# Performance work log

Measured on AMD Instinct MI355X. Metric: run time of the kernel, lower is better.

Reference implementation:

```python
import jax, jax.numpy as jnp
import numpy as np
import math

N_WIRES = 8

def _cnot(state, ctrl, tgt):
    # state: (N, 2,2,...,2) with wire w on axis 1+w
    c_ax = 1 + ctrl
    t_ax = 1 + tgt
    s0 = jnp.take(state, 0, axis=c_ax)
    s1 = jnp.take(state, 1, axis=c_ax)
    t2 = t_ax - 1 if t_ax > c_ax else t_ax
    s1 = jnp.flip(s1, axis=t2)
    return jnp.stack([s0, s1], axis=c_ax)

def _qlayer(x, phi):
    # x: (N, 8) encoder RX angles; phi: (8,) trainable RX angles.
    # encoder RX(x_i) followed by RX(phi_i) on the same wire == RX(x_i + phi_i)
    N = x.shape[0]
    half = 0.5 * (x + phi)
    c = jnp.cos(half).astype(jnp.complex64)
    s = jnp.sin(half).astype(jnp.complex64)
    amp = jnp.stack([c, (-1j) * s], axis=-1)  # (N, 8, 2) per-wire RX|0>
    # product state via successive outer products -> (N, 2,...,2)
    state = amp[:, 0]
    for w in range(1, N_WIRES):
        q = amp[:, w].reshape((N,) + (1,) * w + (2,))
        state = state[..., None] * q
    # CNOT ring
    for w in range(N_WIRES - 1):
        state = _cnot(state, w, w + 1)
    state = _cnot(state, N_WIRES - 1, 0)
    probs = state.real ** 2 + state.imag ** 2  # (N, 2,...,2)
    exps = []
    for w in range(N_WIRES):
        axes = tuple(a for a in range(1, N_WIRES + 1) if a != 1 + w)
        pw = jnp.sum(probs, axis=axes)  # (N, 2)
        exps.append(pw[:, 0] - pw[:, 1])  # <Z_w>
    return jnp.stack(exps, axis=-1)  # (N, 8)


def setup_inputs() -> dict:
    key = jax.random.key(0)
    k1, k2, k3 = jax.random.split(key, 3)
    B, S, E = 4, 1024, 128
    x = jax.random.normal(k1, (B, S, E), jnp.float32)
    phi = jax.random.normal(k2, (N_WIRES,), jnp.float32)
    W = jax.random.normal(k3, (E, E), jnp.float32) / math.sqrt(E)
    b = jnp.zeros((E,), jnp.float32)
    return {"x": x, "phi": phi, "W": W, "b": b}


def reference(x, phi, W, b):
    B, S, E = x.shape
    H = 16
    d = N_WIRES  # head dim == n_wires == 8
    xh = x.reshape(B, S, H, d).reshape(-1, d)
    proj = _qlayer(xh, phi).reshape(B, S, H, d)
    # q, k, v are identical (same layer, same input, deterministic) -> compute once
    q = jnp.transpose(proj, (0, 2, 1, 3))  # (B, H, S, d)
    scores = jnp.einsum('bhqd,bhkd->bhqk', q, q) / math.sqrt(d)
    attn = jax.nn.softmax(scores, axis=-1)  # dropout: eval mode (identity)
    out = jnp.einsum('bhqk,bhkd->bhqd', attn, q)
    out = jnp.transpose(out, (0, 2, 1, 3)).reshape(B, S, E)
    return out @ W.T + b
```

## Files before the change

### kernel.cpp

```cpp
#include <hip/hip_runtime.h>

#define NB 4
#define NS 1024
#define NE 128
#define NH 16
#define ND 8

typedef __attribute__((ext_vector_type(4))) _Float16 half4v;
typedef __attribute__((ext_vector_type(8))) _Float16 half8v;
typedef __attribute__((ext_vector_type(2))) _Float16 half2v;
typedef __attribute__((ext_vector_type(4))) float float4v;

#if __has_builtin(__builtin_amdgcn_exp2f)
#define EXP2F(x) __builtin_amdgcn_exp2f(x)
#else
#define EXP2F(x) __expf(0.69314718055994531f * (x))
#endif

#define SQRT_ALPHA 0.71423656f

__global__ __launch_bounds__(1024, 8)
void qattn_kernel(const float* __restrict__ x, const float* __restrict__ phi,
                  float* __restrict__ aout)
{
    __shared__ __align__(16) _Float16 Klds[NS][8];
    __shared__ __align__(16) _Float16 Vt[9][1036];
    __shared__ __align__(16) float4 scratch[8][64];

    const int t    = threadIdx.x;
    const int blk  = blockIdx.x;
    const int qt   = blk & 7;
    const int bh   = blk >> 3;
    const int b    = bh >> 4;
    const int h    = bh & 15;
    const int lane = t & 63;
    const int w    = t >> 6;
    const int qsub = w & 7;
    const int kh   = w >> 3;

    const float ph0 = phi[0], ph1 = phi[1], ph2 = phi[2], ph3 = phi[3];
    const float ph4 = phi[4], ph5 = phi[5], ph6 = phi[6], ph7 = phi[7];

    {
        const int k = t;
        const float* xr = x + ((size_t)(b * NS + k)) * NE + h * ND;
        float4 xa = *(const float4*)xr;
        float4 xc = *(const float4*)(xr + 4);
        float g0 = __cosf(xa.x + ph0), g1 = __cosf(xa.y + ph1);
        float g2 = __cosf(xa.z + ph2), g3 = __cosf(xa.w + ph3);
        float g4 = __cosf(xc.x + ph4), g5 = __cosf(xc.y + ph5);
        float g6 = __cosf(xc.z + ph6), g7 = __cosf(xc.w + ph7);
        float s7 = g7, s6 = s7 * g6, s5 = s6 * g5, s4 = s5 * g4, s3 = s4 * g3, s2 = s3 * g2;
        float v0 = s2 * g1;
        float v1 = g0 * g1, v2 = v1 * g2, v3 = v2 * g3;
        float v4 = v3 * g4, v5 = v4 * g5, v6 = v5 * g6, v7 = v6 * g7;
        half8v row;
        row[0] = (_Float16)(SQRT_ALPHA * v0); row[1] = (_Float16)(SQRT_ALPHA * v1);
        row[2] = (_Float16)(SQRT_ALPHA * v2); row[3] = (_Float16)(SQRT_ALPHA * v3);
        row[4] = (_Float16)(SQRT_ALPHA * v4); row[5] = (_Float16)(SQRT_ALPHA * v5);
        row[6] = (_Float16)(SQRT_ALPHA * v6); row[7] = (_Float16)(SQRT_ALPHA * v7);
        *(half8v*)&Klds[k][0] = row;
        Vt[0][k] = (_Float16)v0; Vt[1][k] = (_Float16)v1;
        Vt[2][k] = (_Float16)v2; Vt[3][k] = (_Float16)v3;
        Vt[4][k] = (_Float16)v4; Vt[5][k] = (_Float16)v5;
        Vt[6][k] = (_Float16)v6; Vt[7][k] = (_Float16)v7;
        Vt[8][k] = (_Float16)1.0f;
    }
    __syncthreads();

    const int e = lane & 15;
    const int g = lane >> 4;

    half4v qf = (half4v)(_Float16)0.0f;
    if (lane < 32) {
        int qrow = qt * 128 + qsub * 16 + e;
        qf = *(const half4v*)&Klds[qrow][g * 4];
    }

    const _Float16* kp = &Klds[kh * 512 + e][(g & 1) * 4];
    const int ecl = (e > 8) ? 8 : e;
    const _Float16* vp = &Vt[ecl][kh * 512 + g * 4];

    float4v acc = (float4v)0.0f;
    const float4v zero = (float4v)0.0f;

    for (int batch = 0; batch < 8; ++batch) {
        const _Float16* kpb = kp + batch * 512;
        const _Float16* vpb = vp + batch * 64;

        half4v kf0 = *(const half4v*)(kpb);
        half4v kf1 = *(const half4v*)(kpb + 128);
        half4v kf2 = *(const half4v*)(kpb + 256);
        half4v kf3 = *(const half4v*)(kpb + 384);
        half4v vf0 = *(const half4v*)(vpb);
        half4v vf1 = *(const half4v*)(vpb + 16);
        half4v vf2 = *(const half4v*)(vpb + 32);
        half4v vf3 = *(const half4v*)(vpb + 48);

        float4v s0 = __builtin_amdgcn_mfma_f32_16x16x16f16(kf0, qf, zero, 0, 0, 0);
        float4v s1 = __builtin_amdgcn_mfma_f32_16x16x16f16(kf1, qf, zero, 0, 0, 0);
        float4v s2 = __builtin_amdgcn_mfma_f32_16x16x16f16(kf2, qf, zero, 0, 0, 0);
        float4v s3 = __builtin_amdgcn_mfma_f32_16x16x16f16(kf3, qf, zero, 0, 0, 0);

        float p00 = EXP2F(s0[0]), p01 = EXP2F(s0[1]), p02 = EXP2F(s0[2]), p03 = EXP2F(s0[3]);
        float p10 = EXP2F(s1[0]), p11 = EXP2F(s1[1]), p12 = EXP2F(s1[2]), p13 = EXP2F(s1[3]);
        float p20 = EXP2F(s2[0]), p21 = EXP2F(s2[1]), p22 = EXP2F(s2[2]), p23 = EXP2F(s2[3]);
        float p30 = EXP2F(s3[0]), p31 = EXP2F(s3[1]), p32 = EXP2F(s3[2]), p33 = EXP2F(s3[3]);

        half2v lo0 = __builtin_bit_cast(half2v, __builtin_amdgcn_cvt_pkrtz(p00, p01));
        half2v hi0 = __builtin_bit_cast(half2v, __builtin_amdgcn_cvt_pkrtz(p02, p03));
        half2v lo1 = __builtin_bit_cast(half2v, __builtin_amdgcn_cvt_pkrtz(p10, p11));
        half2v hi1 = __builtin_bit_cast(half2v, __builtin_amdgcn_cvt_pkrtz(p12, p13));
        half2v lo2 = __builtin_bit_cast(half2v, __builtin_amdgcn_cvt_pkrtz(p20, p21));
        half2v hi2 = __builtin_bit_cast(half2v, __builtin_amdgcn_cvt_pkrtz(p22, p23));
        half2v lo3 = __builtin_bit_cast(half2v, __builtin_amdgcn_cvt_pkrtz(p30, p31));
        half2v hi3 = __builtin_bit_cast(half2v, __builtin_amdgcn_cvt_pkrtz(p32, p33));
        half4v pa0 = __builtin_shufflevector(lo0, hi0, 0, 1, 2, 3);
        half4v pa1 = __builtin_shufflevector(lo1, hi1, 0, 1, 2, 3);
        half4v pa2 = __builtin_shufflevector(lo2, hi2, 0, 1, 2, 3);
        half4v pa3 = __builtin_shufflevector(lo3, hi3, 0, 1, 2, 3);

        acc = __builtin_amdgcn_mfma_f32_16x16x16f16(pa0, vf0, acc, 0, 0, 0);
        acc = __builtin_amdgcn_mfma_f32_16x16x16f16(pa1, vf1, acc, 0, 0, 0);
        acc = __builtin_amdgcn_mfma_f32_16x16x16f16(pa2, vf2, acc, 0, 0, 0);
        acc = __builtin_amdgcn_mfma_f32_16x16x16f16(pa3, vf3, acc, 0, 0, 0);
    }

    if (kh == 1) {
        scratch[qsub][lane] = make_float4(acc[0], acc[1], acc[2], acc[3]);
    }
    __syncthreads();
    if (kh == 0) {
        float4 c = scratch[qsub][lane];
        acc[0] += c.x; acc[1] += c.y; acc[2] += c.z; acc[3] += c.w;

        const int src = (lane & 48) | 8;
        float d0 = __shfl(acc[0], src, 64);
        float d1 = __shfl(acc[1], src, 64);
        float d2 = __shfl(acc[2], src, 64);
        float d3 = __shfl(acc[3], src, 64);
        float o0 = acc[0] / d0, o1 = acc[1] / d1;
        float o2 = acc[2] / d2, o3 = acc[3] / d3;
        if (e < 8) {
            size_t rbase = (size_t)(b * NS + qt * 128 + qsub * 16 + g * 4);
            float* op = aout + rbase * NE + h * ND + e;
            op[0 * NE] = o0;
            op[1 * NE] = o1;
            op[2 * NE] = o2;
            op[3 * NE] = o3;
        }
    }
}

__global__ __launch_bounds__(512)
void proj_kernel(const float* __restrict__ A, const float* __restrict__ W,
                 const float* __restrict__ bias, float* __restrict__ out)
{
    __shared__ float Wt[64][NE + 4];
    __shared__ float As[16][NE];

    const int t  = threadIdx.x;
    const int r0 = blockIdx.x * 16;

    for (int i = t; i < 16 * NE; i += 512) {
        As[i >> 7][i & 127] = A[(size_t)(r0 + (i >> 7)) * NE + (i & 127)];
    }

    const int c4 = (t & 31) * 4;
    const int rg = t >> 5;
    float acc0 = 0, acc1 = 0, acc2 = 0, acc3 = 0;

    for (int eh = 0; eh < 2; ++eh) {
        if (eh) __syncthreads();
        for (int i = t; i < NE * 64; i += 512) {
            int c = i >> 6;
            int e = i & 63;
            Wt[e][c] = W[c * NE + eh * 64 + e];
        }
        __syncthreads();
#pragma unroll 8
        for (int e = 0; e < 64; ++e) {
            float4 wv = *(const float4*)&Wt[e][c4];
            float av = As[rg][eh * 64 + e];
            acc0 += av * wv.x; acc1 += av * wv.y;
            acc2 += av * wv.z; acc3 += av * wv.w;
        }
    }

    float4 bv = *(const float4*)&bias[c4];
    float4 o = make_float4(acc0 + bv.x, acc1 + bv.y, acc2 + bv.z, acc3 + bv.w);
    *(float4*)(out + (size_t)(r0 + rg) * NE + c4) = o;
}

extern "C" void kernel_launch(void* const* d_in, const int* in_sizes, int n_in,
                              void* d_out, int out_size, void* d_ws, size_t ws_size,
                              hipStream_t stream)
{
    (void)in_sizes; (void)n_in; (void)out_size; (void)d_ws; (void)ws_size;
    const float* x   = (const float*)d_in[0];
    const float* phi = (const float*)d_in[1];
    const float* W   = (const float*)d_in[2];
    const float* b   = (const float*)d_in[3];
    float* out = (float*)d_out;

    qattn_kernel<<<dim3(NB * NH * 8), dim3(1024), 0, stream>>>(x, phi, out);
    proj_kernel<<<dim3(NB * NS / 16), dim3(512), 0, stream>>>(out, W, b, out);
}
```

Before: 24.09 us.

## Halve attention block size and reuse each K/V fragment across four query tiles

The attention kernel now runs 512 threads per block. Each wave handles four 16-row query tiles and one quarter of the keys, so every K and V fragment loaded from LDS feeds four MFMAs instead of one. Each thread computes two key rows in the encoder prologue, and the partial sums from the four key-split waves are combined in two shared-memory reduction steps. This cuts LDS traffic per MFMA but needs more registers per thread and one extra barrier, and each block now has half the waves available to hide latency.

New measurement: 24.86 us. 3.2% more time.

```diff
diff --git a/kernel.cpp b/kernel.cpp
--- a/kernel.cpp
+++ b/kernel.cpp
@@ -19,13 +19,13 @@
 
 #define SQRT_ALPHA 0.71423656f
 
-__global__ __launch_bounds__(1024, 8)
+__global__ __launch_bounds__(512, 4)
 void qattn_kernel(const float* __restrict__ x, const float* __restrict__ phi,
                   float* __restrict__ aout)
 {
     __shared__ __align__(16) _Float16 Klds[NS][8];
     __shared__ __align__(16) _Float16 Vt[9][1036];
-    __shared__ __align__(16) float4 scratch[8][64];
+    __shared__ __align__(16) float4 scratch[2][2][4][64];
 
     const int t    = threadIdx.x;
     const int blk  = blockIdx.x;
@@ -35,72 +35,81 @@
     const int h    = bh & 15;
     const int lane = t & 63;
     const int w    = t >> 6;
-    const int qsub = w & 7;
-    const int kh   = w >> 3;
+    const int qg   = w & 1;
+    const int kh   = w >> 1;
 
     const float ph0 = phi[0], ph1 = phi[1], ph2 = phi[2], ph3 = phi[3];
     const float ph4 = phi[4], ph5 = phi[5], ph6 = phi[6], ph7 = phi[7];
 
     {
-        const int k = t;
-        const float* xr = x + ((size_t)(b * NS + k)) * NE + h * ND;
-        float4 xa = *(const float4*)xr;
-        float4 xc = *(const float4*)(xr + 4);
-        float g0 = __cosf(xa.x + ph0), g1 = __cosf(xa.y + ph1);
-        float g2 = __cosf(xa.z + ph2), g3 = __cosf(xa.w + ph3);
-        float g4 = __cosf(xc.x + ph4), g5 = __cosf(xc.y + ph5);
-        float g6 = __cosf(xc.z + ph6), g7 = __cosf(xc.w + ph7);
-        float s7 = g7, s6 = s7 * g6, s5 = s6 * g5, s4 = s5 * g4, s3 = s4 * g3, s2 = s3 * g2;
-        float v0 = s2 * g1;
-        float v1 = g0 * g1, v2 = v1 * g2, v3 = v2 * g3;
-        float v4 = v3 * g4, v5 = v4 * g5, v6 = v5 * g6, v7 = v6 * g7;
-        half8v row;
-        row[0] = (_Float16)(SQRT_ALPHA * v0); row[1] = (_Float16)(SQRT_ALPHA * v1);
-        row[2] = (_Float16)(SQRT_ALPHA * v2); row[3] = (_Float16)(SQRT_ALPHA * v3);
-        row[4] = (_Float16)(SQRT_ALPHA * v4); row[5] = (_Float16)(SQRT_ALPHA * v5);
-        row[6] = (_Float16)(SQRT_ALPHA * v6); row[7] = (_Float16)(SQRT_ALPHA * v7);
-        *(half8v*)&Klds[k][0] = row;
-        Vt[0][k] = (_Float16)v0; Vt[1][k] = (_Float16)v1;
-        Vt[2][k] = (_Float16)v2; Vt[3][k] = (_Float16)v3;
-        Vt[4][k] = (_Float16)v4; Vt[5][k] = (_Float16)v5;
-        Vt[6][k] = (_Float16)v6; Vt[7][k] = (_Float16)v7;
-        Vt[8][k] = (_Float16)1.0f;
+        const float* xb = x + ((size_t)b * NS) * NE + h * ND;
+        const int k0 = t, k1 = t + 512;
+        float4 xa0 = *(const float4*)(xb + (size_t)k0 * NE);
+        float4 xc0 = *(const float4*)(xb + (size_t)k0 * NE + 4);
+        float4 xa1 = *(const float4*)(xb + (size_t)k1 * NE);
+        float4 xc1 = *(const float4*)(xb + (size_t)k1 * NE + 4);
+#pragma unroll
+        for (int half = 0; half < 2; ++half) {
+            const int k = half ? k1 : k0;
+            const float4 xa = half ? xa1 : xa0;
+            const float4 xc = half ? xc1 : xc0;
+            float g0 = __cosf(xa.x + ph0), g1 = __cosf(xa.y + ph1);
+            float g2 = __cosf(xa.z + ph2), g3 = __cosf(xa.w + ph3);
+            float g4 = __cosf(xc.x + ph4), g5 = __cosf(xc.y + ph5);
+            float g6 = __cosf(xc.z + ph6), g7 = __cosf(xc.w + ph7);
+            float s7 = g7, s6 = s7 * g6, s5 = s6 * g5, s4 = s5 * g4, s3 = s4 * g3, s2 = s3 * g2;
+            float v0 = s2 * g1;
+            float v1 = g0 * g1, v2 = v1 * g2, v3 = v2 * g3;
+            float v4 = v3 * g4, v5 = v4 * g5, v6 = v5 * g6, v7 = v6 * g7;
+            half8v row;
+            row[0] = (_Float16)(SQRT_ALPHA * v0); row[1] = (_Float16)(SQRT_ALPHA * v1);
+            row[2] = (_Float16)(SQRT_ALPHA * v2); row[3] = (_Float16)(SQRT_ALPHA * v3);
+            row[4] = (_Float16)(SQRT_ALPHA * v4); row[5] = (_Float16)(SQRT_ALPHA * v5);
+            row[6] = (_Float16)(SQRT_ALPHA * v6); row[7] = (_Float16)(SQRT_ALPHA * v7);
+            *(half8v*)&Klds[k][0] = row;
+            Vt[0][k] = (_Float16)v0; Vt[1][k] = (_Float16)v1;
+            Vt[2][k] = (_Float16)v2; Vt[3][k] = (_Float16)v3;
+            Vt[4][k] = (_Float16)v4; Vt[5][k] = (_Float16)v5;
+            Vt[6][k] = (_Float16)v6; Vt[7][k] = (_Float16)v7;
+            Vt[8][k] = (_Float16)1.0f;
+        }
     }
     __syncthreads();
 
     const int e = lane & 15;
     const int g = lane >> 4;
 
-    half4v qf = (half4v)(_Float16)0.0f;
+    half4v qf0 = (half4v)(_Float16)0.0f;
+    half4v qf1 = (half4v)(_Float16)0.0f;
+    half4v qf2 = (half4v)(_Float16)0.0f;
+    half4v qf3 = (half4v)(_Float16)0.0f;
     if (lane < 32) {
-        int qrow = qt * 128 + qsub * 16 + e;
-        qf = *(const half4v*)&Klds[qrow][g * 4];
-    }
-
-    const _Float16* kp = &Klds[kh * 512 + e][(g & 1) * 4];
+        const int qbase = qt * 128 + qg * 64 + e;
+        qf0 = *(const half4v*)&Klds[qbase][g * 4];
+        qf1 = *(const half4v*)&Klds[qbase + 16][g * 4];
+        qf2 = *(const half4v*)&Klds[qbase + 32][g * 4];
+        qf3 = *(const half4v*)&Klds[qbase + 48][g * 4];
+    }
+
+    const _Float16* kp = &Klds[kh * 256 + e][(g & 1) * 4];
     const int ecl = (e > 8) ? 8 : e;
-    const _Float16* vp = &Vt[ecl][kh * 512 + g * 4];
-
-    float4v acc = (float4v)0.0f;
+    const _Float16* vp = &Vt[ecl][kh * 256 + g * 4];
+
+    float4v acc0 = (float4v)0.0f;
+    float4v acc1 = (float4v)0.0f;
+    float4v acc2 = (float4v)0.0f;
+    float4v acc3 = (float4v)0.0f;
     const float4v zero = (float4v)0.0f;
 
-    for (int batch = 0; batch < 8; ++batch) {
-        const _Float16* kpb = kp + batch * 512;
-        const _Float16* vpb = vp + batch * 64;
-
-        half4v kf0 = *(const half4v*)(kpb);
-        half4v kf1 = *(const half4v*)(kpb + 128);
-        half4v kf2 = *(const half4v*)(kpb + 256);
-        half4v kf3 = *(const half4v*)(kpb + 384);
-        half4v vf0 = *(const half4v*)(vpb);
-        half4v vf1 = *(const half4v*)(vpb + 16);
-        half4v vf2 = *(const half4v*)(vpb + 32);
-        half4v vf3 = *(const half4v*)(vpb + 48);
-
-        float4v s0 = __builtin_amdgcn_mfma_f32_16x16x16f16(kf0, qf, zero, 0, 0, 0);
-        float4v s1 = __builtin_amdgcn_mfma_f32_16x16x16f16(kf1, qf, zero, 0, 0, 0);
-        float4v s2 = __builtin_amdgcn_mfma_f32_16x16x16f16(kf2, qf, zero, 0, 0, 0);
-        float4v s3 = __builtin_amdgcn_mfma_f32_16x16x16f16(kf3, qf, zero, 0, 0, 0);
+#pragma unroll 4
+    for (int tt = 0; tt < 16; ++tt) {
+        half4v kf = *(const half4v*)(kp + tt * 128);
+        half4v vf = *(const half4v*)(vp + tt * 16);
+
+        float4v s0 = __builtin_amdgcn_mfma_f32_16x16x16f16(kf, qf0, zero, 0, 0, 0);
+        float4v s1 = __builtin_amdgcn_mfma_f32_16x16x16f16(kf, qf1, zero, 0, 0, 0);
+        float4v s2 = __builtin_amdgcn_mfma_f32_16x16x16f16(kf, qf2, zero, 0, 0, 0);
+        float4v s3 = __builtin_amdgcn_mfma_f32_16x16x16f16(kf, qf3, zero, 0, 0, 0);
 
         float p00 = EXP2F(s0[0]), p01 = EXP2F(s0[1]), p02 = EXP2F(s0[2]), p03 = EXP2F(s0[3]);
         float p10 = EXP2F(s1[0]), p11 = EXP2F(s1[1]), p12 = EXP2F(s1[2]), p13 = EXP2F(s1[3]);
@@ -115,39 +124,69 @@
         half2v hi2 = __builtin_bit_cast(half2v, __builtin_amdgcn_cvt_pkrtz(p22, p23));
         half2v lo3 = __builtin_bit_cast(half2v, __builtin_amdgcn_cvt_pkrtz(p30, p31));
         half2v hi3 = __builtin_bit_cast(half2v, __builtin_amdgcn_cvt_pkrtz(p32, p33));
+
         half4v pa0 = __builtin_shufflevector(lo0, hi0, 0, 1, 2, 3);
         half4v pa1 = __builtin_shufflevector(lo1, hi1, 0, 1, 2, 3);
         half4v pa2 = __builtin_shufflevector(lo2, hi2, 0, 1, 2, 3);
         half4v pa3 = __builtin_shufflevector(lo3, hi3, 0, 1, 2, 3);
 
-        acc = __builtin_amdgcn_mfma_f32_16x16x16f16(pa0, vf0, acc, 0, 0, 0);
-        acc = __builtin_amdgcn_mfma_f32_16x16x16f16(pa1, vf1, acc, 0, 0, 0);
-        acc = __builtin_amdgcn_mfma_f32_16x16x16f16(pa2, vf2, acc, 0, 0, 0);
-        acc = __builtin_amdgcn_mfma_f32_16x16x16f16(pa3, vf3, acc, 0, 0, 0);
-    }
-
+        acc0 = __builtin_amdgcn_mfma_f32_16x16x16f16(pa0, vf, acc0, 0, 0, 0);
+        acc1 = __builtin_amdgcn_mfma_f32_16x16x16f16(pa1, vf, acc1, 0, 0, 0);
+        acc2 = __builtin_amdgcn_mfma_f32_16x16x16f16(pa2, vf, acc2, 0, 0, 0);
+        acc3 = __builtin_amdgcn_mfma_f32_16x16x16f16(pa3, vf, acc3, 0, 0, 0);
+    }
+
+    if (kh >= 2) {
+        scratch[kh - 2][qg][0][lane] = make_float4(acc0[0], acc0[1], acc0[2], acc0[3]);
+        scratch[kh - 2][qg][1][lane] = make_float4(acc1[0], acc1[1], acc1[2], acc1[3]);
+        scratch[kh - 2][qg][2][lane] = make_float4(acc2[0], acc2[1], acc2[2], acc2[3]);
+        scratch[kh - 2][qg][3][lane] = make_float4(acc3[0], acc3[1], acc3[2], acc3[3]);
+    }
+    __syncthreads();
+    if (kh < 2) {
+        float4 c0 = scratch[kh][qg][0][lane];
+        float4 c1 = scratch[kh][qg][1][lane];
+        float4 c2 = scratch[kh][qg][2][lane];
+        float4 c3 = scratch[kh][qg][3][lane];
+        acc0[0] += c0.x; acc0[1] += c0.y; acc0[2] += c0.z; acc0[3] += c0.w;
+        acc1[0] += c1.x; acc1[1] += c1.y; acc1[2] += c1.z; acc1[3] += c1.w;
+        acc2[0] += c2.x; acc2[1] += c2.y; acc2[2] += c2.z; acc2[3] += c2.w;
+        acc3[0] += c3.x; acc3[1] += c3.y; acc3[2] += c3.z; acc3[3] += c3.w;
+    }
     if (kh == 1) {
-        scratch[qsub][lane] = make_float4(acc[0], acc[1], acc[2], acc[3]);
+        scratch[1][qg][0][lane] = make_float4(acc0[0], acc0[1], acc0[2], acc0[3]);
+        scratch[1][qg][1][lane] = make_float4(acc1[0], acc1[1], acc1[2], acc1[3]);
+        scratch[1][qg][2][lane] = make_float4(acc2[0], acc2[1], acc2[2], acc2[3]);
+        scratch[1][qg][3][lane] = make_float4(acc3[0], acc3[1], acc3[2], acc3[3]);
     }
     __syncthreads();
     if (kh == 0) {
-        float4 c = scratch[qsub][lane];
-        acc[0] += c.x; acc[1] += c.y; acc[2] += c.z; acc[3] += c.w;
+        float4 c0 = scratch[1][qg][0][lane];
+        float4 c1 = scratch[1][qg][1][lane];
+        float4 c2 = scratch[1][qg][2][lane];
+        float4 c3 = scratch[1][qg][3][lane];
+        acc0[0] += c0.x; acc0[1] += c0.y; acc0[2] += c0.z; acc0[3] += c0.w;
+        acc1[0] += c1.x; acc1[1] += c1.y; acc1[2] += c1.z; acc1[3] += c1.w;
+        acc2[0] += c2.x; acc2[1] += c2.y; acc2[2] += c2.z; acc2[3] += c2.w;
+        acc3[0] += c3.x; acc3[1] += c3.y; acc3[2] += c3.z; acc3[3] += c3.w;
 
         const int src = (lane & 48) | 8;
-        float d0 = __shfl(acc[0], src, 64);
-        float d1 = __shfl(acc[1], src, 64);
-        float d2 = __shfl(acc[2], src, 64);
-        float d3 = __shfl(acc[3], src, 64);
-        float o0 = acc[0] / d0, o1 = acc[1] / d1;
-        float o2 = acc[2] / d2, o3 = acc[3] / d3;
-        if (e < 8) {
-            size_t rbase = (size_t)(b * NS + qt * 128 + qsub * 16 + g * 4);
-            float* op = aout + rbase * NE + h * ND + e;
-            op[0 * NE] = o0;
-            op[1 * NE] = o1;
-            op[2 * NE] = o2;
-            op[3 * NE] = o3;
+        const size_t rb = (size_t)(b * NS + qt * 128 + qg * 64 + g * 4);
+        float* opb = aout + rb * NE + h * ND + e;
+#pragma unroll
+        for (int qs = 0; qs < 4; ++qs) {
+            float4v a = (qs == 0) ? acc0 : (qs == 1) ? acc1 : (qs == 2) ? acc2 : acc3;
+            float d0 = __shfl(a[0], src, 64);
+            float d1 = __shfl(a[1], src, 64);
+            float d2 = __shfl(a[2], src, 64);
+            float d3 = __shfl(a[3], src, 64);
+            if (e < 8) {
+                float* op = opb + (size_t)(qs * 16) * NE;
+                op[0 * NE] = a[0] / d0;
+                op[1 * NE] = a[1] / d1;
+                op[2 * NE] = a[2] / d2;
+                op[3 * NE] = a[3] / d3;
+            }
         }
     }
 }
@@ -203,6 +242,6 @@
     const float* b   = (const float*)d_in[3];
     float* out = (float*)d_out;
 
-    qattn_kernel<<<dim3(NB * NH * 8), dim3(1024), 0, stream>>>(x, phi, out);
+    qattn_kernel<<<dim3(NB * NH * 8), dim3(512), 0, stream>>>(x, phi, out);
     proj_kernel<<<dim3(NB * NS / 16), dim3(512), 0, stream>>>(out, W, b, out);
 }
```
